# Optimization experiments

Hardware: AMD Instinct MI355X
Metric: run time of the kernel (lower is better)

Reference implementation:

```python
import jax, jax.numpy as jnp
import numpy as np
from jax import lax

B, CIN, COUT, K = 256, 3, 16, 3
D, H, W_ = 16, 32, 32
POOL = 4


def setup_inputs() -> dict:
    key = jax.random.key(0)
    kx, kw, kb = jax.random.split(key, 3)
    x = jax.random.normal(kx, (B, CIN, D, H, W_), dtype=jnp.float32)
    # Conv3d default init scale ~ 1/sqrt(fan_in)
    fan_in = CIN * K * K * K
    bound = 1.0 / np.sqrt(fan_in)
    W = jax.random.uniform(kw, (COUT, CIN, K, K, K), dtype=jnp.float32, minval=-bound, maxval=bound)
    b = jax.random.uniform(kb, (COUT,), dtype=jnp.float32, minval=-bound, maxval=bound)
    return {"x": x, "W": W, "b": b}


def reference(x, W, b):
    # Conv3d, valid padding, stride 1: [B,16,14,30,30]
    y = lax.conv_general_dilated(
        x, W, window_strides=(1, 1, 1), padding="VALID",
        dimension_numbers=("NCDHW", "OIDHW", "NCDHW"))
    y = y + b[None, :, None, None, None]
    # channel softmax (dim=1)
    s = jax.nn.softmax(y, axis=1)
    # 4x4x4 max-pool, stride 4, no padding: [B,16,3,7,7]
    out = lax.reduce_window(
        s, -jnp.inf, lax.max,
        window_dimensions=(1, 1, POOL, POOL, POOL),
        window_strides=(1, 1, POOL, POOL, POOL),
        padding="VALID")
    return out
```

## Files before the change

kernel.cpp:

```cpp
#include <hip/hip_runtime.h>
#include <math.h>

#define BATCH 256
#define CIN   3
#define COUT  16
#define DI    16
#define HI    32
#define WI    32

typedef _Float16 f16;
typedef f16   f16x4 __attribute__((ext_vector_type(4)));
typedef f16   f16x8 __attribute__((ext_vector_type(8)));
typedef float f32x4 __attribute__((ext_vector_type(4)));

#define ROWU   144
#define PLANEU 4320
#define XS_N   (6 * PLANEU)
#define G8OFF  (2 * PLANEU + 2 * ROWU)

#define SV8(a, b) __builtin_shufflevector(a, b, 0, 1, 2, 3, 4, 5, 6, 7)
#define MFMA16(A, B, C) __builtin_amdgcn_mfma_f32_16x16x32_f16(A, B, C, 0, 0, 0)

#define CELLD(rb, pmv)  do {                                                  \
    const f16* rb_ = (rb);                                                    \
    f16x4 b10_ = *(const f16x4*)(rb_ + off1);                                 \
    f16x4 b20_ = *(const f16x4*)(rb_ + off2);                                 \
    f16x4 b11_ = *(const f16x4*)(rb_ + off1 + 4);                             \
    f16x4 b21_ = *(const f16x4*)(rb_ + off2 + 4);                             \
    f16x4 b12_ = *(const f16x4*)(rb_ + off1 + 8);                             \
    f16x4 b22_ = *(const f16x4*)(rb_ + off2 + 8);                             \
    f16x4 ga_  = *(const f16x4*)(rb_ + G8OFF + g8sel);                        \
    f16x4 gb_  = *(const f16x4*)(rb_ + G8OFF + g8sel + 4);                    \
    f32x4 a_ = {0.f, 0.f, 0.f, 0.f};                                          \
    a_ = MFMA16(wm[0], SV8(b10_, b20_), a_);                                  \
    a_ = MFMA16(wm[1], SV8(b11_, b21_), a_);                                  \
    a_ = MFMA16(wm[2], SV8(b12_, b22_), a_);                                  \
    a_ = MFMA16(wg,    SV8(ga_,  gb_),  a_);                                  \
    float y0_ = a_[0] + bv.x, y1_ = a_[1] + bv.y;                             \
    float y2_ = a_[2] + bv.z, y3_ = a_[3] + bv.w;                             \
    float e0_ = __expf(y0_), e1_ = __expf(y1_);                               \
    float e2_ = __expf(y2_), e3_ = __expf(y3_);                               \
    float s_ = (e0_ + e1_) + (e2_ + e3_);                                     \
    s_ += __shfl_xor(s_, 16);                                                 \
    s_ += __shfl_xor(s_, 32);                                                 \
    float inv_ = __builtin_amdgcn_rcpf(s_);                                   \
    pmv[0] = fmaxf(pmv[0], e0_ * inv_);                                       \
    pmv[1] = fmaxf(pmv[1], e1_ * inv_);                                       \
    pmv[2] = fmaxf(pmv[2], e2_ * inv_);                                       \
    pmv[3] = fmaxf(pmv[3], e3_ * inv_);                                       \
} while (0)

__global__ __launch_bounds__(256, 3) void conv_sm_pool_mfma(
    const float* __restrict__ x, const float* __restrict__ W,
    const float* __restrict__ bias, float* __restrict__ out)
{
    __shared__ __align__(16) f16 xs[XS_N];

    const int tid  = threadIdx.x;
    const int lane = tid & 63;
    const int wave = tid >> 6;
    const int b    = blockIdx.x / 3;
    const int pd   = blockIdx.x % 3;
    const int d0   = pd * 4;

    const int col = lane & 15;
    const int q   = lane >> 4;

    const float* wc  = W + col * 81;
    const float* wqp = wc + q * 6;
    f16x8 wm[3];
    #pragma unroll
    for (int kw = 0; kw < 3; ++kw) {
        #pragma unroll
        for (int j = 0; j < 8; ++j) {
            const int ci = j & 3, jj = j >> 2;
            float v = (ci < 3) ? wqp[ci * 27 + 3 * jj + kw] : 0.f;
            wm[kw][j] = (f16)v;
        }
    }
    f16x8 wg = {};
    if (q == 0) {
        #pragma unroll
        for (int j = 0; j < 8; ++j) {
            const int ci = j & 3, kw = j >> 2;
            if (ci < 3) wg[j] = (f16)wc[ci * 27 + 24 + kw];
        }
    } else if (q == 1) {
        #pragma unroll
        for (int j = 0; j < 3; ++j) wg[j] = (f16)wc[j * 27 + 26];
    }
    const float4 bv = *(const float4*)(bias + q * 4);

    for (int i = tid; i < 1440; i += 256) {
        int wqd = i & 7;
        int r   = i >> 3;
        int hh  = r % 30;
        int dd  = r / 30;
        const float* px = x + ((size_t)b * 48 + (d0 + dd)) * 1024 + hh * 32 + wqd * 4;
        float4 a0 = *(const float4*)(px);
        float4 a1 = *(const float4*)(px + 16384);
        float4 a2 = *(const float4*)(px + 32768);
        f16x8 p0, p1;
        p0[0] = (f16)a0.x; p0[1] = (f16)a1.x; p0[2] = (f16)a2.x; p0[3] = (f16)0.f;
        p0[4] = (f16)a0.y; p0[5] = (f16)a1.y; p0[6] = (f16)a2.y; p0[7] = (f16)0.f;
        p1[0] = (f16)a0.z; p1[1] = (f16)a1.z; p1[2] = (f16)a2.z; p1[3] = (f16)0.f;
        p1[4] = (f16)a0.w; p1[5] = (f16)a1.w; p1[6] = (f16)a2.w; p1[7] = (f16)0.f;
        f16* dst = xs + ((dd * 30 + hh) * 36 + wqd * 4) * 4;
        *(f16x8*)(dst)     = p0;
        *(f16x8*)(dst + 8) = p1;
    }

    const int g0   = q * 2;
    const int off1 = (g0 / 3) * PLANEU + (g0 % 3) * ROWU;
    const int off2 = ((g0 + 1) / 3) * PLANEU + ((g0 + 1) % 3) * ROWU;
    const int hl = col >> 2, wl = col & 3;
    const int spat  = hl * ROWU + wl * 4;
    const int g8sel = (q == 0) ? 0 : 8;

    __syncthreads();

    for (int c = wave; c < 49; c += 8) {
        const int cA = c;
        int cB = c + 4; if (cB > 48) cB = cA;
        const f16* baseA = xs + (cA / 7) * 4 * ROWU + (cA % 7) * 16 + spat;
        const f16* baseB = xs + (cB / 7) * 4 * ROWU + (cB % 7) * 16 + spat;

        f32x4 pmA = {0.f, 0.f, 0.f, 0.f};
        f32x4 pmB = {0.f, 0.f, 0.f, 0.f};

        #pragma unroll
        for (int d = 0; d < 4; ++d) {
            CELLD(baseA + d * PLANEU, pmA);
            CELLD(baseB + d * PLANEU, pmB);
        }

        #pragma unroll
        for (int m = 1; m <= 8; m <<= 1) {
            pmA[0] = fmaxf(pmA[0], __shfl_xor(pmA[0], m));
            pmA[1] = fmaxf(pmA[1], __shfl_xor(pmA[1], m));
            pmA[2] = fmaxf(pmA[2], __shfl_xor(pmA[2], m));
            pmA[3] = fmaxf(pmA[3], __shfl_xor(pmA[3], m));
            pmB[0] = fmaxf(pmB[0], __shfl_xor(pmB[0], m));
            pmB[1] = fmaxf(pmB[1], __shfl_xor(pmB[1], m));
            pmB[2] = fmaxf(pmB[2], __shfl_xor(pmB[2], m));
            pmB[3] = fmaxf(pmB[3], __shfl_xor(pmB[3], m));
        }

        if (col == 0) {
            float* poA = out + ((size_t)b * COUT + q * 4) * 147 + pd * 49 + cA;
            poA[0]   = pmA[0];
            poA[147] = pmA[1];
            poA[294] = pmA[2];
            poA[441] = pmA[3];
            if (cB != cA) {
                float* poB = out + ((size_t)b * COUT + q * 4) * 147 + pd * 49 + cB;
                poB[0]   = pmB[0];
                poB[147] = pmB[1];
                poB[294] = pmB[2];
                poB[441] = pmB[3];
            }
        }
    }
}

extern "C" void kernel_launch(void* const* d_in, const int* in_sizes, int n_in,
                              void* d_out, int out_size, void* d_ws, size_t ws_size,
                              hipStream_t stream) {
    const float* x    = (const float*)d_in[0];
    const float* W    = (const float*)d_in[1];
    const float* bias = (const float*)d_in[2];
    float* out = (float*)d_out;

    conv_sm_pool_mfma<<<BATCH * 3, 256, 0, stream>>>(x, W, bias, out);
}
```

Baseline: 37.12 us.

## Split each block's width range in two, halve LDS tile, use DPP max reduction

Each (batch, depth-slab) block is split into two blocks that each cover half of the output width, so the shared-memory tile is halved and twice as many blocks launch. The launch bound rises to 8 blocks per CU, aiming for higher occupancy and better latency hiding. Each wave now handles one cell per iteration instead of two. The shuffle-xor max reduction is replaced with DPP row-shift max operations. In exchange, the input columns where the two halves meet are loaded by both blocks, and each wave has less instruction-level parallelism.

After: 38.90 us. 4.8% more time.

```diff
diff --git a/kernel.cpp b/kernel.cpp
--- a/kernel.cpp
+++ b/kernel.cpp
@@ -13,13 +13,19 @@
 typedef f16   f16x8 __attribute__((ext_vector_type(8)));
 typedef float f32x4 __attribute__((ext_vector_type(4)));
 
-#define ROWU   144
-#define PLANEU 4320
-#define XS_N   (6 * PLANEU)
-#define G8OFF  (2 * PLANEU + 2 * ROWU)
+#define RS     72
+#define PLANE  2160
+#define XS_N   (6 * PLANE)
+#define G8OFF  (2 * PLANE + 2 * RS)
 
 #define SV8(a, b) __builtin_shufflevector(a, b, 0, 1, 2, 3, 4, 5, 6, 7)
 #define MFMA16(A, B, C) __builtin_amdgcn_mfma_f32_16x16x32_f16(A, B, C, 0, 0, 0)
+
+#define DPPMAX(v, ctrl) do {                                                  \
+    int t_ = __builtin_amdgcn_update_dpp(                                     \
+        0, __builtin_bit_cast(int, v), (ctrl), 0xF, 0xF, false);              \
+    v = fmaxf(v, __builtin_bit_cast(float, t_));                              \
+} while (0)
 
 #define CELLD(rb, pmv)  do {                                                  \
     const f16* rb_ = (rb);                                                    \
@@ -30,7 +36,7 @@
     f16x4 b12_ = *(const f16x4*)(rb_ + off1 + 8);                             \
     f16x4 b22_ = *(const f16x4*)(rb_ + off2 + 8);                             \
     f16x4 ga_  = *(const f16x4*)(rb_ + G8OFF + g8sel);                        \
-    f16x4 gb_  = *(const f16x4*)(rb_ + G8OFF + g8sel + 4);                    \
+    f16x4 gb_  = *(const f16x4*)(rb_ + G8OFF + 4);                            \
     f32x4 a_ = {0.f, 0.f, 0.f, 0.f};                                          \
     a_ = MFMA16(wm[0], SV8(b10_, b20_), a_);                                  \
     a_ = MFMA16(wm[1], SV8(b11_, b21_), a_);                                  \
@@ -50,7 +56,7 @@
     pmv[3] = fmaxf(pmv[3], e3_ * inv_);                                       \
 } while (0)
 
-__global__ __launch_bounds__(256, 3) void conv_sm_pool_mfma(
+__global__ __launch_bounds__(256, 8) void conv_sm_pool_mfma(
     const float* __restrict__ x, const float* __restrict__ W,
     const float* __restrict__ bias, float* __restrict__ out)
 {
@@ -59,15 +65,18 @@
     const int tid  = threadIdx.x;
     const int lane = tid & 63;
     const int wave = tid >> 6;
-    const int b    = blockIdx.x / 3;
-    const int pd   = blockIdx.x % 3;
+    const int bid  = blockIdx.x;
+    const int cw   = bid & 1;
+    const int bp   = bid >> 1;
+    const int b    = bp / 3;
+    const int pd   = bp % 3;
     const int d0   = pd * 4;
 
     const int col = lane & 15;
-    const int q   = lane >> 4;
+    const int kq  = lane >> 4;
 
     const float* wc  = W + col * 81;
-    const float* wqp = wc + q * 6;
+    const float* wqp = wc + kq * 6;
     f16x8 wm[3];
     #pragma unroll
     for (int kw = 0; kw < 3; ++kw) {
@@ -79,86 +88,93 @@
         }
     }
     f16x8 wg = {};
-    if (q == 0) {
+    if (kq == 0) {
         #pragma unroll
         for (int j = 0; j < 8; ++j) {
             const int ci = j & 3, kw = j >> 2;
             if (ci < 3) wg[j] = (f16)wc[ci * 27 + 24 + kw];
         }
-    } else if (q == 1) {
+    } else if (kq == 1) {
         #pragma unroll
         for (int j = 0; j < 3; ++j) wg[j] = (f16)wc[j * 27 + 26];
     }
-    const float4 bv = *(const float4*)(bias + q * 4);
+    const float4 bv = *(const float4*)(bias + kq * 4);
 
-    for (int i = tid; i < 1440; i += 256) {
-        int wqd = i & 7;
-        int r   = i >> 3;
-        int hh  = r % 30;
-        int dd  = r / 30;
-        const float* px = x + ((size_t)b * 48 + (d0 + dd)) * 1024 + hh * 32 + wqd * 4;
-        float4 a0 = *(const float4*)(px);
-        float4 a1 = *(const float4*)(px + 16384);
-        float4 a2 = *(const float4*)(px + 32768);
-        f16x8 p0, p1;
-        p0[0] = (f16)a0.x; p0[1] = (f16)a1.x; p0[2] = (f16)a2.x; p0[3] = (f16)0.f;
-        p0[4] = (f16)a0.y; p0[5] = (f16)a1.y; p0[6] = (f16)a2.y; p0[7] = (f16)0.f;
-        p1[0] = (f16)a0.z; p1[1] = (f16)a1.z; p1[2] = (f16)a2.z; p1[3] = (f16)0.f;
-        p1[4] = (f16)a0.w; p1[5] = (f16)a1.w; p1[6] = (f16)a2.w; p1[7] = (f16)0.f;
-        f16* dst = xs + ((dd * 30 + hh) * 36 + wqd * 4) * 4;
-        *(f16x8*)(dst)     = p0;
-        *(f16x8*)(dst + 8) = p1;
+    if (cw == 0) {
+        for (int i = tid; i < 900; i += 256) {
+            int q = i % 5, r = i / 5;
+            int hh = r % 30, dd = r / 30;
+            const float* px = x + ((size_t)b * 48 + (d0 + dd)) * 1024 + hh * 32 + q * 4;
+            float4 a0 = *(const float4*)(px);
+            float4 a1 = *(const float4*)(px + 16384);
+            float4 a2 = *(const float4*)(px + 32768);
+            f16x8 p0, p1;
+            p0[0] = (f16)a0.x; p0[1] = (f16)a1.x; p0[2] = (f16)a2.x; p0[3] = (f16)0.f;
+            p0[4] = (f16)a0.y; p0[5] = (f16)a1.y; p0[6] = (f16)a2.y; p0[7] = (f16)0.f;
+            p1[0] = (f16)a0.z; p1[1] = (f16)a1.z; p1[2] = (f16)a2.z; p1[3] = (f16)0.f;
+            p1[4] = (f16)a0.w; p1[5] = (f16)a1.w; p1[6] = (f16)a2.w; p1[7] = (f16)0.f;
+            f16* dst = xs + ((dd * 30 + hh) * 18 + q * 4) * 4;
+            *(f16x8*)(dst) = p0;
+            if (q < 4) *(f16x8*)(dst + 8) = p1;
+        }
+    } else {
+        for (int i = tid; i < 720; i += 256) {
+            int q = i & 3, r = i >> 2;
+            int hh = r % 30, dd = r / 30;
+            const float* px = x + ((size_t)b * 48 + (d0 + dd)) * 1024 + hh * 32 + 16 + q * 4;
+            float4 a0 = *(const float4*)(px);
+            float4 a1 = *(const float4*)(px + 16384);
+            float4 a2 = *(const float4*)(px + 32768);
+            f16x8 p0, p1;
+            p0[0] = (f16)a0.x; p0[1] = (f16)a1.x; p0[2] = (f16)a2.x; p0[3] = (f16)0.f;
+            p0[4] = (f16)a0.y; p0[5] = (f16)a1.y; p0[6] = (f16)a2.y; p0[7] = (f16)0.f;
+            p1[0] = (f16)a0.z; p1[1] = (f16)a1.z; p1[2] = (f16)a2.z; p1[3] = (f16)0.f;
+            p1[4] = (f16)a0.w; p1[5] = (f16)a1.w; p1[6] = (f16)a2.w; p1[7] = (f16)0.f;
+            f16* dst = xs + ((dd * 30 + hh) * 18 + q * 4) * 4;
+            *(f16x8*)(dst)     = p0;
+            *(f16x8*)(dst + 8) = p1;
+        }
     }
 
-    const int g0   = q * 2;
-    const int off1 = (g0 / 3) * PLANEU + (g0 % 3) * ROWU;
-    const int off2 = ((g0 + 1) / 3) * PLANEU + ((g0 + 1) % 3) * ROWU;
+    const int g0   = kq * 2;
+    const int off1 = (g0 / 3) * PLANE + (g0 % 3) * RS;
+    const int off2 = ((g0 + 1) / 3) * PLANE + ((g0 + 1) % 3) * RS;
     const int hl = col >> 2, wl = col & 3;
-    const int spat  = hl * ROWU + wl * 4;
-    const int g8sel = (q == 0) ? 0 : 8;
+    const int spat  = hl * RS + wl * 4;
+    const int g8sel = (kq == 1) ? 8 : 0;
 
     __syncthreads();
 
-    for (int c = wave; c < 49; c += 8) {
-        const int cA = c;
-        int cB = c + 4; if (cB > 48) cB = cA;
-        const f16* baseA = xs + (cA / 7) * 4 * ROWU + (cA % 7) * 16 + spat;
-        const f16* baseB = xs + (cB / 7) * 4 * ROWU + (cB % 7) * 16 + spat;
+    const int ncell = cw ? 21 : 28;
+    for (int c = wave; c < ncell; c += 4) {
+        int ch, pwl;
+        if (cw == 0) { ch = c >> 2; pwl = c & 3; }
+        else         { ch = c / 3;  pwl = c % 3; }
+        const f16* base = xs + ch * 4 * RS + pwl * 16 + spat;
 
-        f32x4 pmA = {0.f, 0.f, 0.f, 0.f};
-        f32x4 pmB = {0.f, 0.f, 0.f, 0.f};
-
+        f32x4 pm = {0.f, 0.f, 0.f, 0.f};
         #pragma unroll
         for (int d = 0; d < 4; ++d) {
-            CELLD(baseA + d * PLANEU, pmA);
-            CELLD(baseB + d * PLANEU, pmB);
+            CELLD(base + d * PLANE, pm);
         }
 
         #pragma unroll
-        for (int m = 1; m <= 8; m <<= 1) {
-            pmA[0] = fmaxf(pmA[0], __shfl_xor(pmA[0], m));
-            pmA[1] = fmaxf(pmA[1], __shfl_xor(pmA[1], m));
-            pmA[2] = fmaxf(pmA[2], __shfl_xor(pmA[2], m));
-            pmA[3] = fmaxf(pmA[3], __shfl_xor(pmA[3], m));
-            pmB[0] = fmaxf(pmB[0], __shfl_xor(pmB[0], m));
-            pmB[1] = fmaxf(pmB[1], __shfl_xor(pmB[1], m));
-            pmB[2] = fmaxf(pmB[2], __shfl_xor(pmB[2], m));
-            pmB[3] = fmaxf(pmB[3], __shfl_xor(pmB[3], m));
+        for (int r = 0; r < 4; ++r) {
+            float v = pm[r];
+            DPPMAX(v, 0x128);
+            DPPMAX(v, 0x124);
+            DPPMAX(v, 0x122);
+            DPPMAX(v, 0x121);
+            pm[r] = v;
         }
 
         if (col == 0) {
-            float* poA = out + ((size_t)b * COUT + q * 4) * 147 + pd * 49 + cA;
-            poA[0]   = pmA[0];
-            poA[147] = pmA[1];
-            poA[294] = pmA[2];
-            poA[441] = pmA[3];
-            if (cB != cA) {
-                float* poB = out + ((size_t)b * COUT + q * 4) * 147 + pd * 49 + cB;
-                poB[0]   = pmB[0];
-                poB[147] = pmB[1];
-                poB[294] = pmB[2];
-                poB[441] = pmB[3];
-            }
+            const int pw = cw ? 4 + pwl : pwl;
+            float* po = out + ((size_t)b * COUT + kq * 4) * 147 + pd * 49 + ch * 7 + pw;
+            po[0]   = pm[0];
+            po[147] = pm[1];
+            po[294] = pm[2];
+            po[441] = pm[3];
         }
     }
 }
@@ -171,5 +187,5 @@
     const float* bias = (const float*)d_in[2];
     float* out = (float*)d_out;
 
-    conv_sm_pool_mfma<<<BATCH * 3, 256, 0, stream>>>(x, W, bias, out);
+    conv_sm_pool_mfma<<<BATCH * 3 * 2, 256, 0, stream>>>(x, W, bias, out);
 }
```
